# Optimization experiments

Measured on AMD Instinct MI355X. Metric: run time of the kernel, lower is better.

The kernel has to match this reference:

```python
import jax, jax.numpy as jnp
import numpy as np

TOP_K = 4


def setup_inputs() -> dict:
    key = jax.random.key(0)
    k1, k2, k3 = jax.random.split(key, 3)
    tokens, hidden_dim, num_experts = 16384, 2880, 128
    hidden_states = jax.random.normal(k1, (tokens, hidden_dim), dtype=jnp.float32)
    weight = jax.random.normal(k2, (num_experts, hidden_dim), dtype=jnp.float32) * 0.02
    bias = jax.random.normal(k3, (num_experts,), dtype=jnp.float32) * 0.02
    return {"hidden_states": hidden_states, "weight": weight, "bias": bias}


def reference(hidden_states, weight, bias):
    # hidden_states: [T, H]; weight: [E, H]; bias: [E]
    x = hidden_states.reshape(-1, weight.shape[1])
    router_logits = jnp.einsum("th,eh->te", x, weight) + bias  # [T, E]
    router_top_value, router_indices = jax.lax.top_k(router_logits, TOP_K)  # [T, K]
    router_top_value = jax.nn.softmax(router_top_value, axis=-1)
    return router_top_value, router_indices, router_logits
```

## Files before the change

### kernel.cpp

```cpp
#include <hip/hip_runtime.h>
#include <math.h>

#define H       2880
#define H4      720
#define NTOK    16384
#define NEXP    128
#define NCHUNK  90
#define NSTEP   180
#define GAP_EPS 1e-3f

typedef __attribute__((ext_vector_type(8)))  short bf16x8;
typedef __attribute__((ext_vector_type(16))) float f32x16;

union FragU { unsigned int u[4]; bf16x8 v; };

__device__ inline bf16x8 pack_hi2(float4 a, float4 b) {
    const float f[8] = {a.x,a.y,a.z,a.w,b.x,b.y,b.z,b.w};
    FragU r;
#pragma unroll
    for (int j = 0; j < 4; ++j) {
        unsigned u0 = __float_as_uint(f[2*j]);
        unsigned u1 = __float_as_uint(f[2*j+1]);
        r.u[j] = (u1 & 0xFFFF0000u) | (u0 >> 16);
    }
    return r.v;
}
__device__ inline bf16x8 pack_lo2(float4 a, float4 b) {
    const float f[8] = {a.x,a.y,a.z,a.w,b.x,b.y,b.z,b.w};
    FragU r;
#pragma unroll
    for (int j = 0; j < 4; ++j) {
        float x0 = f[2*j],   h0 = __uint_as_float(__float_as_uint(x0) & 0xFFFF0000u);
        float x1 = f[2*j+1], h1 = __uint_as_float(__float_as_uint(x1) & 0xFFFF0000u);
        unsigned l0 = __float_as_uint(x0 - h0);
        unsigned l1 = __float_as_uint(x1 - h1);
        r.u[j] = (l1 & 0xFFFF0000u) | (l0 >> 16);
    }
    return r.v;
}

__global__ __launch_bounds__(256) void wconv(
    const float* __restrict__ w, short* __restrict__ whiF, short* __restrict__ wloF)
{
    const int gid = blockIdx.x * 256 + threadIdx.x;
    const int l   = gid & 63;
    const int nt  = (gid >> 6) & 3;
    const int s   = gid >> 8;
    const int e   = nt * 32 + (l & 31);
    const int k0  = s * 16 + (l >> 5) * 8;
    const float4* wp = (const float4*)(w + (size_t)e * H + k0);
    const float4 a = wp[0], b = wp[1];
    *(bf16x8*)(whiF + (size_t)gid * 8) = pack_hi2(a, b);
    *(bf16x8*)(wloF + (size_t)gid * 8) = pack_lo2(a, b);
}

__global__ __launch_bounds__(64, 2) void router_gemm_mfma(
    const float* __restrict__ x,
    const short* __restrict__ whiF,
    const short* __restrict__ wloF,
    float* __restrict__ p0,
    float* __restrict__ pws)
{
    __shared__ float xs[3][1024];

    const int lane = threadIdx.x;
    const int bm   = blockIdx.x;
    const int z    = blockIdx.y;
    const int ks   = gridDim.y;
    const int t0   = bm * 32;

    const int base2 = (NCHUNK / ks) & ~1;
    const int pairs = (NCHUNK - base2 * ks) >> 1;
    const int c0 = z * base2 + 2 * (z < pairs ? z : pairs);
    const int c1 = c0 + base2 + (z < pairs ? 2 : 0);

    float* outp = (z == 0) ? p0 : (pws + (size_t)(z - 1) * NTOK * NEXP);

    const float4* gs = (const float4*)x + (size_t)(t0 + (lane >> 3)) * H4 + ((lane & 7) ^ (lane >> 3));
    const unsigned xsb = (unsigned)(uintptr_t)&xs[0][0];
    const int r31 = lane & 31, lx7 = lane & 7, kh2 = (lane >> 5) * 2;

    f32x16 acc[4];
#pragma unroll
    for (int nt = 0; nt < 4; ++nt)
#pragma unroll
        for (int r = 0; r < 16; ++r) acc[nt][r] = 0.0f;

    bf16x8 bA[16], bB[16];

#define GL(SRC, DST) __builtin_amdgcn_global_load_lds(                                   \
        (const __attribute__((address_space(1))) void*)(SRC),                            \
        (__attribute__((address_space(3))) void*)(DST), 16, 0, 0)

#define STAGE(SB, CC) {                                                                  \
    const float4* g_ = gs + (size_t)(CC) * 8;                                            \
    GL(g_,                  &xs[SB][0]);                                                 \
    GL(g_ + (size_t) 8*H4,  &xs[SB][256]);                                               \
    GL(g_ + (size_t)16*H4,  &xs[SB][512]);                                               \
    GL(g_ + (size_t)24*H4,  &xs[SB][768]); }

#define BLOAD_ST(DST, CC, ST) {                                                          \
    _Pragma("unroll")                                                                    \
    for (int nt = 0; nt < 4; ++nt) {                                                     \
        const size_t o_ = ((size_t)(((CC)*2 + (ST))*4 + nt)*64 + lane) * 8;              \
        DST[(ST)*8 + nt*2]     = *(const bf16x8*)(whiF + o_);                            \
        DST[(ST)*8 + nt*2 + 1] = *(const bf16x8*)(wloF + o_); } }

#define MFMA_HALF(BANK, ST, AH, AL) {                                                    \
    _Pragma("unroll")                                                                    \
    for (int nt = 0; nt < 4; ++nt) {                                                     \
        acc[nt] = __builtin_amdgcn_mfma_f32_32x32x16_bf16(AH, BANK[(ST)*8 + nt*2],     acc[nt], 0,0,0); \
        acc[nt] = __builtin_amdgcn_mfma_f32_32x32x16_bf16(AL, BANK[(ST)*8 + nt*2],     acc[nt], 0,0,0); \
        acc[nt] = __builtin_amdgcn_mfma_f32_32x32x16_bf16(AH, BANK[(ST)*8 + nt*2 + 1], acc[nt], 0,0,0); } }

#define DSREAD_PACK(BUF, AH0, AL0, AH1, AL1) {                                           \
    const unsigned ab  = xsb + (unsigned)(BUF) * 4096u + (unsigned)r31 * 128u;           \
    const unsigned a00 = ab + 16u * (unsigned)((kh2    ) ^ lx7);                         \
    const unsigned a01 = ab + 16u * (unsigned)((kh2 + 1) ^ lx7);                         \
    const unsigned a10 = ab + 16u * (unsigned)((kh2 + 4) ^ lx7);                         \
    const unsigned a11 = ab + 16u * (unsigned)((kh2 + 5) ^ lx7);                         \
    float4 q0, q1, q2, q3;                                                               \
    asm volatile("ds_read_b128 %0, %1" : "=v"(q0) : "v"(a00) : "memory");                \
    asm volatile("ds_read_b128 %0, %1" : "=v"(q1) : "v"(a01) : "memory");                \
    asm volatile("ds_read_b128 %0, %1" : "=v"(q2) : "v"(a10) : "memory");                \
    asm volatile("ds_read_b128 %0, %1" : "=v"(q3) : "v"(a11) : "memory");                \
    asm volatile("s_waitcnt lgkmcnt(0)" ::: "memory");                                   \
    __builtin_amdgcn_sched_barrier(0);                                                   \
    AH0 = pack_hi2(q0, q1); AL0 = pack_lo2(q0, q1);                                      \
    AH1 = pack_hi2(q2, q3); AL1 = pack_lo2(q2, q3); }

    STAGE(0, c0);
    STAGE(1, c0 + 1);
    BLOAD_ST(bA, c0, 0);     BLOAD_ST(bA, c0, 1);
    BLOAD_ST(bB, c0 + 1, 0); BLOAD_ST(bB, c0 + 1, 1);

    int rb = 0;
    bf16x8 ah0, al0, ah1, al1;
    for (int c = c0; c < c1 - 2; c += 2) {
        const int sb  = (rb + 2 >= 3) ? rb - 1 : rb + 2;
        const int rb1 = (rb + 1 >= 3) ? 0 : rb + 1;
        STAGE(sb, c + 2);
        asm volatile("s_waitcnt vmcnt(40)" ::: "memory");
        DSREAD_PACK(rb, ah0, al0, ah1, al1);
        MFMA_HALF(bA, 0, ah0, al0);
        BLOAD_ST(bA, c + 2, 0);
        MFMA_HALF(bA, 1, ah1, al1);
        BLOAD_ST(bA, c + 2, 1);
        STAGE(rb, c + 3);
        asm volatile("s_waitcnt vmcnt(40)" ::: "memory");
        DSREAD_PACK(rb1, ah0, al0, ah1, al1);
        MFMA_HALF(bB, 0, ah0, al0);
        BLOAD_ST(bB, c + 3, 0);
        MFMA_HALF(bB, 1, ah1, al1);
        BLOAD_ST(bB, c + 3, 1);
        rb = (rb >= 1) ? rb - 1 : 2;
    }
    {
        const int rb1 = (rb + 1 >= 3) ? 0 : rb + 1;
        asm volatile("s_waitcnt vmcnt(36)" ::: "memory");
        DSREAD_PACK(rb, ah0, al0, ah1, al1);
        MFMA_HALF(bA, 0, ah0, al0);
        MFMA_HALF(bA, 1, ah1, al1);
        asm volatile("s_waitcnt vmcnt(16)" ::: "memory");
        DSREAD_PACK(rb1, ah0, al0, ah1, al1);
        MFMA_HALF(bB, 0, ah0, al0);
        MFMA_HALF(bB, 1, ah1, al1);
    }

    const int ecol  = lane & 31;
    const int rbase = t0 + 4 * (lane >> 5);
#pragma unroll
    for (int nt = 0; nt < 4; ++nt)
#pragma unroll
        for (int r = 0; r < 16; ++r) {
            const int orow = rbase + (r & 3) + 8 * (r >> 2);
            outp[(size_t)orow * NEXP + nt * 32 + ecol] = acc[nt][r];
        }
}

__global__ __launch_bounds__(256) void reduce_cand(
    float* __restrict__ p0,
    const float* __restrict__ pws,
    const float* __restrict__ bias,
    int* __restrict__ cand,
    float* __restrict__ vals,
    float* __restrict__ inds,
    int ks)
{
    const int tid = threadIdx.x;
    const int tok = blockIdx.x * 8 + (tid >> 5);
    const int l   = tid & 31;

    float4* row = (float4*)p0 + (size_t)tok * 32 + l;
    float4 s = row[0];
    for (int zz = 1; zz < ks; ++zz) {
        const float4 pz = ((const float4*)(pws + (size_t)(zz - 1) * NTOK * NEXP))[(size_t)tok * 32 + l];
        s.x += pz.x; s.y += pz.y; s.z += pz.z; s.w += pz.w;
    }
    const float4 bb = ((const float4*)bias)[l];
    s.x += bb.x; s.y += bb.y; s.z += bb.z; s.w += bb.w;
    row[0] = s;

    float v[4] = {s.x, s.y, s.z, s.w};
    float vv[8]; int out[8];
#pragma unroll
    for (int r = 0; r < 8; ++r) {
        float lv = v[0]; int lj = 0;
#pragma unroll
        for (int j = 1; j < 4; ++j) if (v[j] > lv) { lv = v[j]; lj = j; }
        int le = l * 4 + lj;
#pragma unroll
        for (int m = 1; m < 32; m <<= 1) {
            const float ov = __shfl_xor(lv, m, 32);
            const int   oe = __shfl_xor(le, m, 32);
            if (ov > lv || (ov == lv && oe < le)) { lv = ov; le = oe; }
        }
        vv[r] = lv; out[r] = le;
        if ((le >> 2) == l) v[le & 3] = -3.4e38f;
    }

    float ming = vv[0] - vv[1];
    ming = fminf(ming, vv[1] - vv[2]);
    ming = fminf(ming, vv[2] - vv[3]);
    ming = fminf(ming, vv[3] - vv[4]);
    const bool slow = (ming < GAP_EPS);

    if (l == 0) {
        int4 o0 = {out[0] | (slow ? (1 << 30) : 0), out[1], out[2], out[3]};
        int4 o1 = {out[4], out[5], out[6], out[7]};
        *(int4*)(cand + (size_t)tok * 8)     = o0;
        *(int4*)(cand + (size_t)tok * 8 + 4) = o1;
        if (!slow) {
            const float e1 = expf(vv[1] - vv[0]);
            const float e2 = expf(vv[2] - vv[0]);
            const float e3 = expf(vv[3] - vv[0]);
            const float sm = 1.0f + e1 + e2 + e3;
            float4 ov = {1.0f / sm, e1 / sm, e2 / sm, e3 / sm};
            float4 oi = {(float)out[0], (float)out[1], (float)out[2], (float)out[3]};
            *(float4*)(&vals[(size_t)tok * 4]) = ov;
            *(float4*)(&inds[(size_t)tok * 4]) = oi;
        }
    }
}

__global__ __launch_bounds__(256) void fixup_topk(
    const float* __restrict__ x,
    const float* __restrict__ w,
    const float* __restrict__ bias,
    const int* __restrict__ cand,
    float* __restrict__ vals,
    float* __restrict__ inds)
{
    const int lane = threadIdx.x & 63;
    const int wv   = threadIdx.x >> 6;
    const int tok  = blockIdx.x * 4 + wv;

    const int head = cand[(size_t)tok * 8];
    if (!(head & (1 << 30))) return;

    const int c    = lane >> 3;
    const int s    = lane & 7;
    const int cidx = cand[(size_t)tok * 8 + c] & 0x3fffffff;

    const float4* xr = (const float4*)x + (size_t)tok  * H4;
    const float4* wr = (const float4*)w + (size_t)cidx * H4;

    double acc = 0.0;
    for (int j = 0; j < 90; ++j) {
        const float4 a = xr[s + 8 * j];
        const float4 b = wr[s + 8 * j];
        acc = fma((double)a.x, (double)b.x, acc);
        acc = fma((double)a.y, (double)b.y, acc);
        acc = fma((double)a.z, (double)b.z, acc);
        acc = fma((double)a.w, (double)b.w, acc);
    }
    acc += __shfl_xor(acc, 1);
    acc += __shfl_xor(acc, 2);
    acc += __shfl_xor(acc, 4);
    const double exact = acc + (double)bias[cidx];

    double bv[8]; int bidx[8];
#pragma unroll
    for (int g = 0; g < 8; ++g) { bv[g] = __shfl(exact, g * 8); bidx[g] = __shfl(cidx, g * 8); }

    float fv[4]; int fi[4];
#pragma unroll
    for (int k = 0; k < 4; ++k) {
        double best = -1.0e300; int bi = 1 << 30; int bg = -1;
#pragma unroll
        for (int g = 0; g < 8; ++g) {
            if (bv[g] > best || (bv[g] == best && bidx[g] < bi)) { best = bv[g]; bi = bidx[g]; bg = g; }
        }
#pragma unroll
        for (int g = 0; g < 8; ++g) if (g == bg) bv[g] = -1.0e300;
        fv[k] = (float)best; fi[k] = bi;
    }

    if (lane == 0) {
        const float e1 = expf(fv[1] - fv[0]);
        const float e2 = expf(fv[2] - fv[0]);
        const float e3 = expf(fv[3] - fv[0]);
        const float sm = 1.0f + e1 + e2 + e3;
        float4 ov = {1.0f / sm, e1 / sm, e2 / sm, e3 / sm};
        float4 oi = {(float)fi[0], (float)fi[1], (float)fi[2], (float)fi[3]};
        *(float4*)(&vals[(size_t)tok * 4]) = ov;
        *(float4*)(&inds[(size_t)tok * 4]) = oi;
    }
}

extern "C" void kernel_launch(void* const* d_in, const int* in_sizes, int n_in,
                              void* d_out, int out_size, void* d_ws, size_t ws_size,
                              hipStream_t stream) {
    const float* x    = (const float*)d_in[0];
    const float* w    = (const float*)d_in[1];
    const float* bias = (const float*)d_in[2];

    float* out    = (float*)d_out;
    float* vals   = out;
    float* inds   = out + NTOK * 4;
    float* logits = out + NTOK * 8;

    const size_t WPLANE = (size_t)NEXP * H * sizeof(short);
    const size_t PB     = (size_t)NTOK * NEXP * sizeof(float);
    const size_t CB     = (size_t)NTOK * 8 * sizeof(int);

    int ks = 1;
    if      (ws_size >= 2 * WPLANE + 3 * PB + CB) ks = 4;
    else if (ws_size >= 2 * WPLANE + 1 * PB + CB) ks = 2;

    short* whiF = (short*)d_ws;
    short* wloF = whiF + (size_t)NEXP * H;
    float* pws  = (float*)(wloF + (size_t)NEXP * H);
    int*   cand = (int*)(pws + (size_t)(ks - 1) * NTOK * NEXP);

    wconv<<<NSTEP, 256, 0, stream>>>(w, whiF, wloF);
    router_gemm_mfma<<<dim3(NTOK / 32, ks), 64, 0, stream>>>(x, whiF, wloF, logits, pws);
    reduce_cand<<<NTOK / 8, 256, 0, stream>>>(logits, pws, bias, cand, vals, inds, ks);
    fixup_topk<<<NTOK / 4, 256, 0, stream>>>(x, w, bias, cand, vals, inds);
}
```

Measured before the change: 85.65 us.

## Split GEMM expert columns across blocks and fuse reduce with exact fixup

The router GEMM now gives each block half of the experts (64 columns), which halves the accumulator and weight-register footprint. In exchange the launch bound rises to 3 waves and LDS staging drops from triple to double buffering. The K split changes from 4 to 3, and the candidate-reduction and fp64 fixup kernels merge into one kernel, removing the candidate buffer round trip and one launch. The activation tile is now loaded twice, once per expert half. A leftover dead kernel, reduce_fix, is defined but never launched.

```diff
diff --git a/kernel.cpp b/kernel.cpp
--- a/kernel.cpp
+++ b/kernel.cpp
@@ -54,17 +54,19 @@
     *(bf16x8*)(wloF + (size_t)gid * 8) = pack_lo2(a, b);
 }
 
-__global__ __launch_bounds__(64, 2) void router_gemm_mfma(
+__global__ __launch_bounds__(64, 3) void router_gemm_mfma(
     const float* __restrict__ x,
     const short* __restrict__ whiF,
     const short* __restrict__ wloF,
     float* __restrict__ p0,
     float* __restrict__ pws)
 {
-    __shared__ float xs[3][1024];
+    __shared__ float xs[2][1024];
 
     const int lane = threadIdx.x;
-    const int bm   = blockIdx.x;
+    const int bx   = blockIdx.x;
+    const int bm   = bx >> 1;
+    const int eh   = bx & 1;
     const int z    = blockIdx.y;
     const int ks   = gridDim.y;
     const int t0   = bm * 32;
@@ -80,13 +82,11 @@
     const unsigned xsb = (unsigned)(uintptr_t)&xs[0][0];
     const int r31 = lane & 31, lx7 = lane & 7, kh2 = (lane >> 5) * 2;
 
-    f32x16 acc[4];
-#pragma unroll
-    for (int nt = 0; nt < 4; ++nt)
-#pragma unroll
-        for (int r = 0; r < 16; ++r) acc[nt][r] = 0.0f;
-
-    bf16x8 bA[16], bB[16];
+    f32x16 acc0, acc1;
+#pragma unroll
+    for (int r = 0; r < 16; ++r) { acc0[r] = 0.0f; acc1[r] = 0.0f; }
+
+    bf16x8 bA[8], bB[8];
 
 #define GL(SRC, DST) __builtin_amdgcn_global_load_lds(                                   \
         (const __attribute__((address_space(1))) void*)(SRC),                            \
@@ -101,17 +101,18 @@
 
 #define BLOAD_ST(DST, CC, ST) {                                                          \
     _Pragma("unroll")                                                                    \
-    for (int nt = 0; nt < 4; ++nt) {                                                     \
-        const size_t o_ = ((size_t)(((CC)*2 + (ST))*4 + nt)*64 + lane) * 8;              \
-        DST[(ST)*8 + nt*2]     = *(const bf16x8*)(whiF + o_);                            \
-        DST[(ST)*8 + nt*2 + 1] = *(const bf16x8*)(wloF + o_); } }
-
-#define MFMA_HALF(BANK, ST, AH, AL) {                                                    \
-    _Pragma("unroll")                                                                    \
-    for (int nt = 0; nt < 4; ++nt) {                                                     \
-        acc[nt] = __builtin_amdgcn_mfma_f32_32x32x16_bf16(AH, BANK[(ST)*8 + nt*2],     acc[nt], 0,0,0); \
-        acc[nt] = __builtin_amdgcn_mfma_f32_32x32x16_bf16(AL, BANK[(ST)*8 + nt*2],     acc[nt], 0,0,0); \
-        acc[nt] = __builtin_amdgcn_mfma_f32_32x32x16_bf16(AH, BANK[(ST)*8 + nt*2 + 1], acc[nt], 0,0,0); } }
+    for (int nt = 0; nt < 2; ++nt) {                                                     \
+        const size_t o_ = ((size_t)(((CC)*2 + (ST))*4 + eh*2 + nt)*64 + lane) * 8;       \
+        DST[(ST)*4 + nt*2]     = *(const bf16x8*)(whiF + o_);                            \
+        DST[(ST)*4 + nt*2 + 1] = *(const bf16x8*)(wloF + o_); } }
+
+#define MFMA_ST(BANK, ST, AH, AL) {                                                      \
+    acc0 = __builtin_amdgcn_mfma_f32_32x32x16_bf16(AH, BANK[(ST)*4 + 0], acc0, 0,0,0);   \
+    acc0 = __builtin_amdgcn_mfma_f32_32x32x16_bf16(AL, BANK[(ST)*4 + 0], acc0, 0,0,0);   \
+    acc0 = __builtin_amdgcn_mfma_f32_32x32x16_bf16(AH, BANK[(ST)*4 + 1], acc0, 0,0,0);   \
+    acc1 = __builtin_amdgcn_mfma_f32_32x32x16_bf16(AH, BANK[(ST)*4 + 2], acc1, 0,0,0);   \
+    acc1 = __builtin_amdgcn_mfma_f32_32x32x16_bf16(AL, BANK[(ST)*4 + 2], acc1, 0,0,0);   \
+    acc1 = __builtin_amdgcn_mfma_f32_32x32x16_bf16(AH, BANK[(ST)*4 + 3], acc1, 0,0,0); }
 
 #define DSREAD_PACK(BUF, AH0, AL0, AH1, AL1) {                                           \
     const unsigned ab  = xsb + (unsigned)(BUF) * 4096u + (unsigned)r31 * 128u;           \
@@ -130,59 +131,54 @@
     AH1 = pack_hi2(q2, q3); AL1 = pack_lo2(q2, q3); }
 
     STAGE(0, c0);
+    BLOAD_ST(bA, c0, 0);     BLOAD_ST(bA, c0, 1);
     STAGE(1, c0 + 1);
-    BLOAD_ST(bA, c0, 0);     BLOAD_ST(bA, c0, 1);
     BLOAD_ST(bB, c0 + 1, 0); BLOAD_ST(bB, c0 + 1, 1);
 
-    int rb = 0;
     bf16x8 ah0, al0, ah1, al1;
     for (int c = c0; c < c1 - 2; c += 2) {
-        const int sb  = (rb + 2 >= 3) ? rb - 1 : rb + 2;
-        const int rb1 = (rb + 1 >= 3) ? 0 : rb + 1;
-        STAGE(sb, c + 2);
-        asm volatile("s_waitcnt vmcnt(40)" ::: "memory");
-        DSREAD_PACK(rb, ah0, al0, ah1, al1);
-        MFMA_HALF(bA, 0, ah0, al0);
+        asm volatile("s_waitcnt vmcnt(20)" ::: "memory");
+        DSREAD_PACK(0, ah0, al0, ah1, al1);
+        STAGE(0, c + 2);
+        MFMA_ST(bA, 0, ah0, al0);
         BLOAD_ST(bA, c + 2, 0);
-        MFMA_HALF(bA, 1, ah1, al1);
+        MFMA_ST(bA, 1, ah1, al1);
         BLOAD_ST(bA, c + 2, 1);
-        STAGE(rb, c + 3);
-        asm volatile("s_waitcnt vmcnt(40)" ::: "memory");
-        DSREAD_PACK(rb1, ah0, al0, ah1, al1);
-        MFMA_HALF(bB, 0, ah0, al0);
+
+        asm volatile("s_waitcnt vmcnt(20)" ::: "memory");
+        DSREAD_PACK(1, ah0, al0, ah1, al1);
+        STAGE(1, c + 3);
+        MFMA_ST(bB, 0, ah0, al0);
         BLOAD_ST(bB, c + 3, 0);
-        MFMA_HALF(bB, 1, ah1, al1);
+        MFMA_ST(bB, 1, ah1, al1);
         BLOAD_ST(bB, c + 3, 1);
-        rb = (rb >= 1) ? rb - 1 : 2;
     }
     {
-        const int rb1 = (rb + 1 >= 3) ? 0 : rb + 1;
-        asm volatile("s_waitcnt vmcnt(36)" ::: "memory");
-        DSREAD_PACK(rb, ah0, al0, ah1, al1);
-        MFMA_HALF(bA, 0, ah0, al0);
-        MFMA_HALF(bA, 1, ah1, al1);
-        asm volatile("s_waitcnt vmcnt(16)" ::: "memory");
-        DSREAD_PACK(rb1, ah0, al0, ah1, al1);
-        MFMA_HALF(bB, 0, ah0, al0);
-        MFMA_HALF(bB, 1, ah1, al1);
-    }
-
-    const int ecol  = lane & 31;
+        asm volatile("s_waitcnt vmcnt(20)" ::: "memory");
+        DSREAD_PACK(0, ah0, al0, ah1, al1);
+        MFMA_ST(bA, 0, ah0, al0);
+        MFMA_ST(bA, 1, ah1, al1);
+        asm volatile("s_waitcnt vmcnt(8)" ::: "memory");
+        DSREAD_PACK(1, ah0, al0, ah1, al1);
+        MFMA_ST(bB, 0, ah0, al0);
+        MFMA_ST(bB, 1, ah1, al1);
+    }
+
+    const int ecol  = eh * 64 + (lane & 31);
     const int rbase = t0 + 4 * (lane >> 5);
 #pragma unroll
-    for (int nt = 0; nt < 4; ++nt)
-#pragma unroll
-        for (int r = 0; r < 16; ++r) {
-            const int orow = rbase + (r & 3) + 8 * (r >> 2);
-            outp[(size_t)orow * NEXP + nt * 32 + ecol] = acc[nt][r];
-        }
-}
-
-__global__ __launch_bounds__(256) void reduce_cand(
+    for (int r = 0; r < 16; ++r) {
+        const int orow = rbase + (r & 3) + 8 * (r >> 2);
+        outp[(size_t)orow * NEXP + ecol]      = acc0[r];
+        outp[(size_t)orow * NEXP + ecol + 32] = acc1[r];
+    }
+}
+
+__global__ __launch_bounds__(256) void reduce_fix(
+    const float* __restrict__ x,
     float* __restrict__ p0,
     const float* __restrict__ pws,
     const float* __restrict__ bias,
-    int* __restrict__ cand,
     float* __restrict__ vals,
     float* __restrict__ inds,
     int ks)
@@ -202,7 +198,7 @@
     row[0] = s;
 
     float v[4] = {s.x, s.y, s.z, s.w};
-    float vv[8]; int out[8];
+    float vv[8]; int out8[8];
 #pragma unroll
     for (int r = 0; r < 8; ++r) {
         float lv = v[0]; int lj = 0;
@@ -215,7 +211,7 @@
             const int   oe = __shfl_xor(le, m, 32);
             if (ov > lv || (ov == lv && oe < le)) { lv = ov; le = oe; }
         }
-        vv[r] = lv; out[r] = le;
+        vv[r] = lv; out8[r] = le;
         if ((le >> 2) == l) v[le & 3] = -3.4e38f;
     }
 
@@ -223,52 +219,108 @@
     ming = fminf(ming, vv[1] - vv[2]);
     ming = fminf(ming, vv[2] - vv[3]);
     ming = fminf(ming, vv[3] - vv[4]);
-    const bool slow = (ming < GAP_EPS);
-
-    if (l == 0) {
-        int4 o0 = {out[0] | (slow ? (1 << 30) : 0), out[1], out[2], out[3]};
-        int4 o1 = {out[4], out[5], out[6], out[7]};
-        *(int4*)(cand + (size_t)tok * 8)     = o0;
-        *(int4*)(cand + (size_t)tok * 8 + 4) = o1;
-        if (!slow) {
+
+    if (ming >= GAP_EPS) {
+        if (l == 0) {
             const float e1 = expf(vv[1] - vv[0]);
             const float e2 = expf(vv[2] - vv[0]);
             const float e3 = expf(vv[3] - vv[0]);
             const float sm = 1.0f + e1 + e2 + e3;
             float4 ov = {1.0f / sm, e1 / sm, e2 / sm, e3 / sm};
-            float4 oi = {(float)out[0], (float)out[1], (float)out[2], (float)out[3]};
+            float4 oi = {(float)out8[0], (float)out8[1], (float)out8[2], (float)out8[3]};
             *(float4*)(&vals[(size_t)tok * 4]) = ov;
             *(float4*)(&inds[(size_t)tok * 4]) = oi;
         }
-    }
-}
-
-__global__ __launch_bounds__(256) void fixup_topk(
+        return;
+    }
+
+    const int cslot = l >> 2;
+    const int q     = l & 3;
+    int cidx = out8[0];
+#pragma unroll
+    for (int g = 1; g < 8; ++g) if (cslot == g) cidx = out8[g];
+
+    const float4* xr = (const float4*)x + (size_t)tok  * H4;
+    const float4* wr4 = (const float4*)0;
+    {
+    }
+    (void)wr4;
+}
+
+__global__ __launch_bounds__(256) void reduce_fix_w(
     const float* __restrict__ x,
     const float* __restrict__ w,
+    float* __restrict__ p0,
+    const float* __restrict__ pws,
     const float* __restrict__ bias,
-    const int* __restrict__ cand,
     float* __restrict__ vals,
-    float* __restrict__ inds)
+    float* __restrict__ inds,
+    int ks)
 {
-    const int lane = threadIdx.x & 63;
-    const int wv   = threadIdx.x >> 6;
-    const int tok  = blockIdx.x * 4 + wv;
-
-    const int head = cand[(size_t)tok * 8];
-    if (!(head & (1 << 30))) return;
-
-    const int c    = lane >> 3;
-    const int s    = lane & 7;
-    const int cidx = cand[(size_t)tok * 8 + c] & 0x3fffffff;
+    const int tid = threadIdx.x;
+    const int tok = blockIdx.x * 8 + (tid >> 5);
+    const int l   = tid & 31;
+
+    float4* row = (float4*)p0 + (size_t)tok * 32 + l;
+    float4 s = row[0];
+    for (int zz = 1; zz < ks; ++zz) {
+        const float4 pz = ((const float4*)(pws + (size_t)(zz - 1) * NTOK * NEXP))[(size_t)tok * 32 + l];
+        s.x += pz.x; s.y += pz.y; s.z += pz.z; s.w += pz.w;
+    }
+    const float4 bb = ((const float4*)bias)[l];
+    s.x += bb.x; s.y += bb.y; s.z += bb.z; s.w += bb.w;
+    row[0] = s;
+
+    float v[4] = {s.x, s.y, s.z, s.w};
+    float vv[8]; int out8[8];
+#pragma unroll
+    for (int r = 0; r < 8; ++r) {
+        float lv = v[0]; int lj = 0;
+#pragma unroll
+        for (int j = 1; j < 4; ++j) if (v[j] > lv) { lv = v[j]; lj = j; }
+        int le = l * 4 + lj;
+#pragma unroll
+        for (int m = 1; m < 32; m <<= 1) {
+            const float ov = __shfl_xor(lv, m, 32);
+            const int   oe = __shfl_xor(le, m, 32);
+            if (ov > lv || (ov == lv && oe < le)) { lv = ov; le = oe; }
+        }
+        vv[r] = lv; out8[r] = le;
+        if ((le >> 2) == l) v[le & 3] = -3.4e38f;
+    }
+
+    float ming = vv[0] - vv[1];
+    ming = fminf(ming, vv[1] - vv[2]);
+    ming = fminf(ming, vv[2] - vv[3]);
+    ming = fminf(ming, vv[3] - vv[4]);
+
+    if (ming >= GAP_EPS) {
+        if (l == 0) {
+            const float e1 = expf(vv[1] - vv[0]);
+            const float e2 = expf(vv[2] - vv[0]);
+            const float e3 = expf(vv[3] - vv[0]);
+            const float sm = 1.0f + e1 + e2 + e3;
+            float4 ov = {1.0f / sm, e1 / sm, e2 / sm, e3 / sm};
+            float4 oi = {(float)out8[0], (float)out8[1], (float)out8[2], (float)out8[3]};
+            *(float4*)(&vals[(size_t)tok * 4]) = ov;
+            *(float4*)(&inds[(size_t)tok * 4]) = oi;
+        }
+        return;
+    }
+
+    const int cslot = l >> 2;
+    const int q     = l & 3;
+    int cidx = out8[0];
+#pragma unroll
+    for (int g = 1; g < 8; ++g) if (cslot == g) cidx = out8[g];
 
     const float4* xr = (const float4*)x + (size_t)tok  * H4;
     const float4* wr = (const float4*)w + (size_t)cidx * H4;
 
     double acc = 0.0;
-    for (int j = 0; j < 90; ++j) {
-        const float4 a = xr[s + 8 * j];
-        const float4 b = wr[s + 8 * j];
+    for (int j = 0; j < 180; ++j) {
+        const float4 a = xr[q + 4 * j];
+        const float4 b = wr[q + 4 * j];
         acc = fma((double)a.x, (double)b.x, acc);
         acc = fma((double)a.y, (double)b.y, acc);
         acc = fma((double)a.z, (double)b.z, acc);
@@ -276,12 +328,15 @@
     }
     acc += __shfl_xor(acc, 1);
     acc += __shfl_xor(acc, 2);
-    acc += __shfl_xor(acc, 4);
     const double exact = acc + (double)bias[cidx];
 
+    const int base = tid & 32;
     double bv[8]; int bidx[8];
 #pragma unroll
-    for (int g = 0; g < 8; ++g) { bv[g] = __shfl(exact, g * 8); bidx[g] = __shfl(cidx, g * 8); }
+    for (int g = 0; g < 8; ++g) {
+        bv[g]   = __shfl(exact, base + g * 4);
+        bidx[g] = __shfl(cidx,  base + g * 4);
+    }
 
     float fv[4]; int fi[4];
 #pragma unroll
@@ -296,7 +351,7 @@
         fv[k] = (float)best; fi[k] = bi;
     }
 
-    if (lane == 0) {
+    if (l == 0) {
         const float e1 = expf(fv[1] - fv[0]);
         const float e2 = expf(fv[2] - fv[0]);
         const float e3 = expf(fv[3] - fv[0]);
@@ -322,19 +377,15 @@
 
     const size_t WPLANE = (size_t)NEXP * H * sizeof(short);
     const size_t PB     = (size_t)NTOK * NEXP * sizeof(float);
-    const size_t CB     = (size_t)NTOK * 8 * sizeof(int);
 
     int ks = 1;
-    if      (ws_size >= 2 * WPLANE + 3 * PB + CB) ks = 4;
-    else if (ws_size >= 2 * WPLANE + 1 * PB + CB) ks = 2;
+    if (ws_size >= 2 * WPLANE + 2 * PB) ks = 3;
 
     short* whiF = (short*)d_ws;
     short* wloF = whiF + (size_t)NEXP * H;
     float* pws  = (float*)(wloF + (size_t)NEXP * H);
-    int*   cand = (int*)(pws + (size_t)(ks - 1) * NTOK * NEXP);
 
     wconv<<<NSTEP, 256, 0, stream>>>(w, whiF, wloF);
-    router_gemm_mfma<<<dim3(NTOK / 32, ks), 64, 0, stream>>>(x, whiF, wloF, logits, pws);
-    reduce_cand<<<NTOK / 8, 256, 0, stream>>>(logits, pws, bias, cand, vals, inds, ks);
-    fixup_topk<<<NTOK / 4, 256, 0, stream>>>(x, w, bias, cand, vals, inds);
-}
+    router_gemm_mfma<<<dim3(NTOK / 32 * 2, ks), 64, 0, stream>>>(x, whiF, wloF, logits, pws);
+    reduce_fix_w<<<NTOK / 8, 256, 0, stream>>>(x, w, logits, pws, bias, vals, inds, ks);
+}
```

New measurement: 135.1 us. 1.58x slower.

## Pack four waves per GEMM block, widen split-K, fuse fixup into reduce

Applied to the files above, without the earlier changes.

The GEMM block now holds four independent waves, each with its own double-buffered LDS region. This replaces the single-wave triple-buffer rotation with a fixed two-buffer scheme and a different wait count. Split-K can grow to 6 or 8 when the workspace allows it. The separate fixup kernel and the candidate buffer are removed: the reduce kernel computes the exact fp64 dot products in place for ambiguous tokens, which saves one launch and one round trip of intermediate data. The costs are more partial-sum traffic at higher split-K and divergent fp64 work inside the reduce kernel.

```diff
diff --git a/kernel.cpp b/kernel.cpp
--- a/kernel.cpp
+++ b/kernel.cpp
@@ -54,17 +54,19 @@
     *(bf16x8*)(wloF + (size_t)gid * 8) = pack_lo2(a, b);
 }
 
-__global__ __launch_bounds__(64, 2) void router_gemm_mfma(
+__global__ __launch_bounds__(256, 2) void router_gemm_mfma(
     const float* __restrict__ x,
     const short* __restrict__ whiF,
     const short* __restrict__ wloF,
     float* __restrict__ p0,
     float* __restrict__ pws)
 {
-    __shared__ float xs[3][1024];
-
-    const int lane = threadIdx.x;
-    const int bm   = blockIdx.x;
+    __shared__ float xs[4][2][1024];
+
+    const int tid  = threadIdx.x;
+    const int lane = tid & 63;
+    const int wv   = tid >> 6;
+    const int bm   = blockIdx.x * 4 + wv;
     const int z    = blockIdx.y;
     const int ks   = gridDim.y;
     const int t0   = bm * 32;
@@ -77,7 +79,7 @@
     float* outp = (z == 0) ? p0 : (pws + (size_t)(z - 1) * NTOK * NEXP);
 
     const float4* gs = (const float4*)x + (size_t)(t0 + (lane >> 3)) * H4 + ((lane & 7) ^ (lane >> 3));
-    const unsigned xsb = (unsigned)(uintptr_t)&xs[0][0];
+    const unsigned xsb = (unsigned)(uintptr_t)&xs[wv][0][0];
     const int r31 = lane & 31, lx7 = lane & 7, kh2 = (lane >> 5) * 2;
 
     f32x16 acc[4];
@@ -94,10 +96,10 @@
 
 #define STAGE(SB, CC) {                                                                  \
     const float4* g_ = gs + (size_t)(CC) * 8;                                            \
-    GL(g_,                  &xs[SB][0]);                                                 \
-    GL(g_ + (size_t) 8*H4,  &xs[SB][256]);                                               \
-    GL(g_ + (size_t)16*H4,  &xs[SB][512]);                                               \
-    GL(g_ + (size_t)24*H4,  &xs[SB][768]); }
+    GL(g_,                  &xs[wv][SB][0]);                                             \
+    GL(g_ + (size_t) 8*H4,  &xs[wv][SB][256]);                                           \
+    GL(g_ + (size_t)16*H4,  &xs[wv][SB][512]);                                           \
+    GL(g_ + (size_t)24*H4,  &xs[wv][SB][768]); }
 
 #define BLOAD_ST(DST, CC, ST) {                                                          \
     _Pragma("unroll")                                                                    \
@@ -106,7 +108,7 @@
         DST[(ST)*8 + nt*2]     = *(const bf16x8*)(whiF + o_);                            \
         DST[(ST)*8 + nt*2 + 1] = *(const bf16x8*)(wloF + o_); } }
 
-#define MFMA_HALF(BANK, ST, AH, AL) {                                                    \
+#define MFMA_ST(BANK, ST, AH, AL) {                                                      \
     _Pragma("unroll")                                                                    \
     for (int nt = 0; nt < 4; ++nt) {                                                     \
         acc[nt] = __builtin_amdgcn_mfma_f32_32x32x16_bf16(AH, BANK[(ST)*8 + nt*2],     acc[nt], 0,0,0); \
@@ -130,41 +132,37 @@
     AH1 = pack_hi2(q2, q3); AL1 = pack_lo2(q2, q3); }
 
     STAGE(0, c0);
+    BLOAD_ST(bA, c0, 0);     BLOAD_ST(bA, c0, 1);
     STAGE(1, c0 + 1);
-    BLOAD_ST(bA, c0, 0);     BLOAD_ST(bA, c0, 1);
     BLOAD_ST(bB, c0 + 1, 0); BLOAD_ST(bB, c0 + 1, 1);
 
-    int rb = 0;
     bf16x8 ah0, al0, ah1, al1;
     for (int c = c0; c < c1 - 2; c += 2) {
-        const int sb  = (rb + 2 >= 3) ? rb - 1 : rb + 2;
-        const int rb1 = (rb + 1 >= 3) ? 0 : rb + 1;
-        STAGE(sb, c + 2);
-        asm volatile("s_waitcnt vmcnt(40)" ::: "memory");
-        DSREAD_PACK(rb, ah0, al0, ah1, al1);
-        MFMA_HALF(bA, 0, ah0, al0);
+        asm volatile("s_waitcnt vmcnt(36)" ::: "memory");
+        DSREAD_PACK(0, ah0, al0, ah1, al1);
+        STAGE(0, c + 2);
+        MFMA_ST(bA, 0, ah0, al0);
         BLOAD_ST(bA, c + 2, 0);
-        MFMA_HALF(bA, 1, ah1, al1);
+        MFMA_ST(bA, 1, ah1, al1);
         BLOAD_ST(bA, c + 2, 1);
-        STAGE(rb, c + 3);
-        asm volatile("s_waitcnt vmcnt(40)" ::: "memory");
-        DSREAD_PACK(rb1, ah0, al0, ah1, al1);
-        MFMA_HALF(bB, 0, ah0, al0);
+
+        asm volatile("s_waitcnt vmcnt(36)" ::: "memory");
+        DSREAD_PACK(1, ah0, al0, ah1, al1);
+        STAGE(1, c + 3);
+        MFMA_ST(bB, 0, ah0, al0);
         BLOAD_ST(bB, c + 3, 0);
-        MFMA_HALF(bB, 1, ah1, al1);
+        MFMA_ST(bB, 1, ah1, al1);
         BLOAD_ST(bB, c + 3, 1);
-        rb = (rb >= 1) ? rb - 1 : 2;
     }
     {
-        const int rb1 = (rb + 1 >= 3) ? 0 : rb + 1;
         asm volatile("s_waitcnt vmcnt(36)" ::: "memory");
-        DSREAD_PACK(rb, ah0, al0, ah1, al1);
-        MFMA_HALF(bA, 0, ah0, al0);
-        MFMA_HALF(bA, 1, ah1, al1);
+        DSREAD_PACK(0, ah0, al0, ah1, al1);
+        MFMA_ST(bA, 0, ah0, al0);
+        MFMA_ST(bA, 1, ah1, al1);
         asm volatile("s_waitcnt vmcnt(16)" ::: "memory");
-        DSREAD_PACK(rb1, ah0, al0, ah1, al1);
-        MFMA_HALF(bB, 0, ah0, al0);
-        MFMA_HALF(bB, 1, ah1, al1);
+        DSREAD_PACK(1, ah0, al0, ah1, al1);
+        MFMA_ST(bB, 0, ah0, al0);
+        MFMA_ST(bB, 1, ah1, al1);
     }
 
     const int ecol  = lane & 31;
@@ -178,11 +176,12 @@
         }
 }
 
-__global__ __launch_bounds__(256) void reduce_cand(
+__global__ __launch_bounds__(256) void reduce_fix(
+    const float* __restrict__ x,
+    const float* __restrict__ w,
     float* __restrict__ p0,
     const float* __restrict__ pws,
     const float* __restrict__ bias,
-    int* __restrict__ cand,
     float* __restrict__ vals,
     float* __restrict__ inds,
     int ks)
@@ -202,7 +201,7 @@
     row[0] = s;
 
     float v[4] = {s.x, s.y, s.z, s.w};
-    float vv[8]; int out[8];
+    float vv[8]; int out8[8];
 #pragma unroll
     for (int r = 0; r < 8; ++r) {
         float lv = v[0]; int lj = 0;
@@ -215,7 +214,7 @@
             const int   oe = __shfl_xor(le, m, 32);
             if (ov > lv || (ov == lv && oe < le)) { lv = ov; le = oe; }
         }
-        vv[r] = lv; out[r] = le;
+        vv[r] = lv; out8[r] = le;
         if ((le >> 2) == l) v[le & 3] = -3.4e38f;
     }
 
@@ -223,52 +222,34 @@
     ming = fminf(ming, vv[1] - vv[2]);
     ming = fminf(ming, vv[2] - vv[3]);
     ming = fminf(ming, vv[3] - vv[4]);
-    const bool slow = (ming < GAP_EPS);
-
-    if (l == 0) {
-        int4 o0 = {out[0] | (slow ? (1 << 30) : 0), out[1], out[2], out[3]};
-        int4 o1 = {out[4], out[5], out[6], out[7]};
-        *(int4*)(cand + (size_t)tok * 8)     = o0;
-        *(int4*)(cand + (size_t)tok * 8 + 4) = o1;
-        if (!slow) {
+
+    if (ming >= GAP_EPS) {
+        if (l == 0) {
             const float e1 = expf(vv[1] - vv[0]);
             const float e2 = expf(vv[2] - vv[0]);
             const float e3 = expf(vv[3] - vv[0]);
             const float sm = 1.0f + e1 + e2 + e3;
             float4 ov = {1.0f / sm, e1 / sm, e2 / sm, e3 / sm};
-            float4 oi = {(float)out[0], (float)out[1], (float)out[2], (float)out[3]};
+            float4 oi = {(float)out8[0], (float)out8[1], (float)out8[2], (float)out8[3]};
             *(float4*)(&vals[(size_t)tok * 4]) = ov;
             *(float4*)(&inds[(size_t)tok * 4]) = oi;
         }
-    }
-}
-
-__global__ __launch_bounds__(256) void fixup_topk(
-    const float* __restrict__ x,
-    const float* __restrict__ w,
-    const float* __restrict__ bias,
-    const int* __restrict__ cand,
-    float* __restrict__ vals,
-    float* __restrict__ inds)
-{
-    const int lane = threadIdx.x & 63;
-    const int wv   = threadIdx.x >> 6;
-    const int tok  = blockIdx.x * 4 + wv;
-
-    const int head = cand[(size_t)tok * 8];
-    if (!(head & (1 << 30))) return;
-
-    const int c    = lane >> 3;
-    const int s    = lane & 7;
-    const int cidx = cand[(size_t)tok * 8 + c] & 0x3fffffff;
+        return;
+    }
+
+    const int cslot = l >> 2;
+    const int q     = l & 3;
+    int cidx = out8[0];
+#pragma unroll
+    for (int g = 1; g < 8; ++g) if (cslot == g) cidx = out8[g];
 
     const float4* xr = (const float4*)x + (size_t)tok  * H4;
     const float4* wr = (const float4*)w + (size_t)cidx * H4;
 
     double acc = 0.0;
-    for (int j = 0; j < 90; ++j) {
-        const float4 a = xr[s + 8 * j];
-        const float4 b = wr[s + 8 * j];
+    for (int j = 0; j < 180; ++j) {
+        const float4 a = xr[q + 4 * j];
+        const float4 b = wr[q + 4 * j];
         acc = fma((double)a.x, (double)b.x, acc);
         acc = fma((double)a.y, (double)b.y, acc);
         acc = fma((double)a.z, (double)b.z, acc);
@@ -276,12 +257,15 @@
     }
     acc += __shfl_xor(acc, 1);
     acc += __shfl_xor(acc, 2);
-    acc += __shfl_xor(acc, 4);
     const double exact = acc + (double)bias[cidx];
 
+    const int base = tid & 32;
     double bv[8]; int bidx[8];
 #pragma unroll
-    for (int g = 0; g < 8; ++g) { bv[g] = __shfl(exact, g * 8); bidx[g] = __shfl(cidx, g * 8); }
+    for (int g = 0; g < 8; ++g) {
+        bv[g]   = __shfl(exact, base + g * 4);
+        bidx[g] = __shfl(cidx,  base + g * 4);
+    }
 
     float fv[4]; int fi[4];
 #pragma unroll
@@ -296,7 +280,7 @@
         fv[k] = (float)best; fi[k] = bi;
     }
 
-    if (lane == 0) {
+    if (l == 0) {
         const float e1 = expf(fv[1] - fv[0]);
         const float e2 = expf(fv[2] - fv[0]);
         const float e3 = expf(fv[3] - fv[0]);
@@ -322,19 +306,18 @@
 
     const size_t WPLANE = (size_t)NEXP * H * sizeof(short);
     const size_t PB     = (size_t)NTOK * NEXP * sizeof(float);
-    const size_t CB     = (size_t)NTOK * 8 * sizeof(int);
 
     int ks = 1;
-    if      (ws_size >= 2 * WPLANE + 3 * PB + CB) ks = 4;
-    else if (ws_size >= 2 * WPLANE + 1 * PB + CB) ks = 2;
+    if      (ws_size >= 2 * WPLANE + 7 * PB) ks = 8;
+    else if (ws_size >= 2 * WPLANE + 5 * PB) ks = 6;
+    else if (ws_size >= 2 * WPLANE + 3 * PB) ks = 4;
+    else if (ws_size >= 2 * WPLANE + 1 * PB) ks = 2;
 
     short* whiF = (short*)d_ws;
     short* wloF = whiF + (size_t)NEXP * H;
     float* pws  = (float*)(wloF + (size_t)NEXP * H);
-    int*   cand = (int*)(pws + (size_t)(ks - 1) * NTOK * NEXP);
 
     wconv<<<NSTEP, 256, 0, stream>>>(w, whiF, wloF);
-    router_gemm_mfma<<<dim3(NTOK / 32, ks), 64, 0, stream>>>(x, whiF, wloF, logits, pws);
-    reduce_cand<<<NTOK / 8, 256, 0, stream>>>(logits, pws, bias, cand, vals, inds, ks);
-    fixup_topk<<<NTOK / 4, 256, 0, stream>>>(x, w, bias, cand, vals, inds);
-}
+    router_gemm_mfma<<<dim3(NTOK / 32 / 4, ks), 256, 0, stream>>>(x, whiF, wloF, logits, pws);
+    reduce_fix<<<NTOK / 8, 256, 0, stream>>>(x, w, logits, pws, bias, vals, inds, ks);
+}
```

New measurement: 143.2 us. 1.67x slower.

## Deepen x staging pipeline from three to four LDS buffers

Applied to the files above, without the earlier changes.

Grows the shared-memory ring for x tiles from 3 to 4 buffers and restructures the main loop with an explicit prologue and epilogue, so each chunk's global load is issued further ahead of its use. The vmcnt waits are retuned so more loads stay in flight. This aims to hide more global-memory latency. The cost is more LDS per block, which may reduce occupancy, and the hand-set waitcnt values risk being wrong for some chunk counts.

```diff
diff --git a/kernel.cpp b/kernel.cpp
--- a/kernel.cpp
+++ b/kernel.cpp
@@ -61,7 +61,7 @@
     float* __restrict__ p0,
     float* __restrict__ pws)
 {
-    __shared__ float xs[3][1024];
+    __shared__ float xs[4][1024];
 
     const int lane = threadIdx.x;
     const int bm   = blockIdx.x;
@@ -131,41 +131,84 @@
 
     STAGE(0, c0);
     STAGE(1, c0 + 1);
+    STAGE(2, c0 + 2);
     BLOAD_ST(bA, c0, 0);     BLOAD_ST(bA, c0, 1);
     BLOAD_ST(bB, c0 + 1, 0); BLOAD_ST(bB, c0 + 1, 1);
 
+    bf16x8 ah0, al0, ah1, al1;
+
+    STAGE(3, c0 + 3);
+    asm volatile("s_waitcnt vmcnt(44)" ::: "memory");
+    DSREAD_PACK(0, ah0, al0, ah1, al1);
+    MFMA_HALF(bA, 0, ah0, al0);
+    BLOAD_ST(bA, c0 + 2, 0);
+    MFMA_HALF(bA, 1, ah1, al1);
+    BLOAD_ST(bA, c0 + 2, 1);
+    STAGE(0, c0 + 4);
+    asm volatile("s_waitcnt vmcnt(60)" ::: "memory");
+    DSREAD_PACK(1, ah0, al0, ah1, al1);
+    MFMA_HALF(bB, 0, ah0, al0);
+    BLOAD_ST(bB, c0 + 3, 0);
+    MFMA_HALF(bB, 1, ah1, al1);
+    BLOAD_ST(bB, c0 + 3, 1);
+
+    STAGE(1, c0 + 5);
+    asm volatile("s_waitcnt vmcnt(63)" ::: "memory");
+    DSREAD_PACK(2, ah0, al0, ah1, al1);
+    MFMA_HALF(bA, 0, ah0, al0);
+    BLOAD_ST(bA, c0 + 4, 0);
+    MFMA_HALF(bA, 1, ah1, al1);
+    BLOAD_ST(bA, c0 + 4, 1);
+    STAGE(2, c0 + 6);
+    asm volatile("s_waitcnt vmcnt(60)" ::: "memory");
+    DSREAD_PACK(3, ah0, al0, ah1, al1);
+    MFMA_HALF(bB, 0, ah0, al0);
+    BLOAD_ST(bB, c0 + 5, 0);
+    MFMA_HALF(bB, 1, ah1, al1);
+    BLOAD_ST(bB, c0 + 5, 1);
+
     int rb = 0;
-    bf16x8 ah0, al0, ah1, al1;
-    for (int c = c0; c < c1 - 2; c += 2) {
-        const int sb  = (rb + 2 >= 3) ? rb - 1 : rb + 2;
-        const int rb1 = (rb + 1 >= 3) ? 0 : rb + 1;
-        STAGE(sb, c + 2);
-        asm volatile("s_waitcnt vmcnt(40)" ::: "memory");
+    for (int c = c0 + 4; c < c1 - 4; c += 2) {
+        STAGE(rb ^ 3, c + 3);
+        asm volatile("s_waitcnt vmcnt(60)" ::: "memory");
         DSREAD_PACK(rb, ah0, al0, ah1, al1);
         MFMA_HALF(bA, 0, ah0, al0);
         BLOAD_ST(bA, c + 2, 0);
         MFMA_HALF(bA, 1, ah1, al1);
         BLOAD_ST(bA, c + 2, 1);
-        STAGE(rb, c + 3);
-        asm volatile("s_waitcnt vmcnt(40)" ::: "memory");
-        DSREAD_PACK(rb1, ah0, al0, ah1, al1);
+        STAGE(rb, c + 4);
+        asm volatile("s_waitcnt vmcnt(60)" ::: "memory");
+        DSREAD_PACK(rb + 1, ah0, al0, ah1, al1);
         MFMA_HALF(bB, 0, ah0, al0);
         BLOAD_ST(bB, c + 3, 0);
         MFMA_HALF(bB, 1, ah1, al1);
         BLOAD_ST(bB, c + 3, 1);
-        rb = (rb >= 1) ? rb - 1 : 2;
-    }
-    {
-        const int rb1 = (rb + 1 >= 3) ? 0 : rb + 1;
-        asm volatile("s_waitcnt vmcnt(36)" ::: "memory");
-        DSREAD_PACK(rb, ah0, al0, ah1, al1);
-        MFMA_HALF(bA, 0, ah0, al0);
-        MFMA_HALF(bA, 1, ah1, al1);
-        asm volatile("s_waitcnt vmcnt(16)" ::: "memory");
-        DSREAD_PACK(rb1, ah0, al0, ah1, al1);
-        MFMA_HALF(bB, 0, ah0, al0);
-        MFMA_HALF(bB, 1, ah1, al1);
-    }
+        rb ^= 2;
+    }
+
+    STAGE(rb ^ 3, c1 - 1);
+    asm volatile("s_waitcnt vmcnt(60)" ::: "memory");
+    DSREAD_PACK(rb, ah0, al0, ah1, al1);
+    MFMA_HALF(bA, 0, ah0, al0);
+    BLOAD_ST(bA, c1 - 2, 0);
+    MFMA_HALF(bA, 1, ah1, al1);
+    BLOAD_ST(bA, c1 - 2, 1);
+    asm volatile("s_waitcnt vmcnt(56)" ::: "memory");
+    DSREAD_PACK(rb + 1, ah0, al0, ah1, al1);
+    MFMA_HALF(bB, 0, ah0, al0);
+    BLOAD_ST(bB, c1 - 1, 0);
+    MFMA_HALF(bB, 1, ah1, al1);
+    BLOAD_ST(bB, c1 - 1, 1);
+    rb ^= 2;
+
+    asm volatile("s_waitcnt vmcnt(52)" ::: "memory");
+    DSREAD_PACK(rb, ah0, al0, ah1, al1);
+    MFMA_HALF(bA, 0, ah0, al0);
+    MFMA_HALF(bA, 1, ah1, al1);
+    asm volatile("s_waitcnt vmcnt(32)" ::: "memory");
+    DSREAD_PACK(rb + 1, ah0, al0, ah1, al1);
+    MFMA_HALF(bB, 0, ah0, al0);
+    MFMA_HALF(bB, 1, ah1, al1);
 
     const int ecol  = lane & 31;
     const int rbase = t0 + 4 * (lane >> 5);
@@ -178,6 +221,7 @@
         }
 }
 
+#define INSERTX(v, e)
 __global__ __launch_bounds__(256) void reduce_cand(
     float* __restrict__ p0,
     const float* __restrict__ pws,
```

Measured after the change: 86.31 us. About the same (+0.8%).
